# Performance work log

Hardware: AMD Instinct MI355X
Metric: run time of the kernel (lower is better)

## Reference

```python
import jax, jax.numpy as jnp
import numpy as np
from jax import lax

MODEL_DIM = 256
CTX_LEN = 48
CHUNK = 16
NUM_LAYERS = 4
NHEAD = 8
FF_DIM = 1024
EPS = 1e-5


def setup_inputs() -> dict:
    key = jax.random.key(0)
    ks = jax.random.split(key, 16)
    B, C, T = 16, MODEL_DIM, 1024
    s = 0.02
    inp = {
        "x": jax.random.normal(ks[0], (B, C, T), dtype=jnp.float32),
        "embedding": jax.random.normal(ks[1], (B, 2, C, 32), dtype=jnp.float32),
        "ctx_buf": jnp.zeros((B, NUM_LAYERS, CTX_LEN, C), dtype=jnp.float32),
        # per-layer stacked transformer-decoder-layer params
        "Wqkv": jax.random.normal(ks[2], (NUM_LAYERS, 3 * C, C), dtype=jnp.float32) * s,
        "bqkv": jnp.zeros((NUM_LAYERS, 3 * C), dtype=jnp.float32),
        "Wo": jax.random.normal(ks[3], (NUM_LAYERS, C, C), dtype=jnp.float32) * s,
        "bo": jnp.zeros((NUM_LAYERS, C), dtype=jnp.float32),
        "W1": jax.random.normal(ks[4], (NUM_LAYERS, FF_DIM, C), dtype=jnp.float32) * s,
        "b1": jnp.zeros((NUM_LAYERS, FF_DIM), dtype=jnp.float32),
        "W2": jax.random.normal(ks[5], (NUM_LAYERS, C, FF_DIM), dtype=jnp.float32) * s,
        "b2": jnp.zeros((NUM_LAYERS, C), dtype=jnp.float32),
        "ln1_g": jnp.ones((NUM_LAYERS, C), dtype=jnp.float32),
        "ln1_b": jnp.zeros((NUM_LAYERS, C), dtype=jnp.float32),
        "ln3_g": jnp.ones((NUM_LAYERS, C), dtype=jnp.float32),
        "ln3_b": jnp.zeros((NUM_LAYERS, C), dtype=jnp.float32),
    }
    return inp


def _layernorm(x, g, b):
    mu = jnp.mean(x, axis=-1, keepdims=True)
    var = jnp.mean(jnp.square(x - mu), axis=-1, keepdims=True)
    return (x - mu) * lax.rsqrt(var + EPS) * g + b


def _mha(q_in, kv_in, Wqkv, bqkv, Wo, bo):
    # q_in: [N, Lq, C], kv_in: [N, Lk, C]; torch nn.MultiheadAttention math (eval mode)
    C = q_in.shape[-1]
    dh = C // NHEAD
    Wq, Wk, Wv = jnp.split(Wqkv, 3, axis=0)
    bq, bk, bv = jnp.split(bqkv, 3)
    q = q_in @ Wq.T + bq
    k = kv_in @ Wk.T + bk
    v = kv_in @ Wv.T + bv
    N, Lq, _ = q.shape
    Lk = k.shape[1]
    q = q.reshape(N, Lq, NHEAD, dh)
    k = k.reshape(N, Lk, NHEAD, dh)
    v = v.reshape(N, Lk, NHEAD, dh)
    scores = jnp.einsum("nqhd,nkhd->nhqk", q, k) / jnp.sqrt(jnp.asarray(dh, q.dtype))
    attn = jax.nn.softmax(scores, axis=-1)
    out = jnp.einsum("nhqk,nkhd->nqhd", attn, v).reshape(N, Lq, C)
    return out @ Wo.T + bo


def _decoder_layer(tgt, Wqkv, bqkv, Wo, bo, W1, b1, W2, b2, ln1_g, ln1_b, ln3_g, ln3_b):
    # tgt: [N, ctx+chunk, C]; query = last `chunk` tokens; dropout=identity (eval)
    q = tgt[:, -CHUNK:, :]
    x1 = _layernorm(q + _mha(q, tgt, Wqkv, bqkv, Wo, bo), ln1_g, ln1_b)
    ff = jax.nn.relu(x1 @ W1.T + b1) @ W2.T + b2
    return _layernorm(x1 + ff, ln3_g, ln3_b)


def reference(x, embedding, ctx_buf, Wqkv, bqkv, Wo, bo, W1, b1, W2, b2,
              ln1_g, ln1_b, ln3_g, ln3_b):
    B, C, T = x.shape  # T multiple of CHUNK -> mod_pad is a no-op
    # ---- conv conditioning: per-(batch,channel) causal depthwise filter ----
    Le = embedding.shape[-1]
    filt = jnp.mean(embedding, axis=1).reshape(B * C, 1, Le)  # [B*C, 1, Le]
    inp = x.reshape(1, B * C, T)
    out = lax.conv_general_dilated(
        inp, filt, window_strides=(1,), padding=[(Le - 1, 0)],
        feature_group_count=B * C, dimension_numbers=("NCH", "OIH", "NCH"))
    output = out.reshape(B, C, T).transpose(0, 2, 1)  # [B, T, C]

    # ---- causal sliding-window decoder layers ----
    nwin = T // CHUNK
    W = CTX_LEN + CHUNK
    idx = jnp.arange(nwin)[:, None] * CHUNK + jnp.arange(W)[None, :]  # [nwin, W]
    for i in range(NUM_LAYERS):
        tgt_full = jnp.concatenate([ctx_buf[:, i], output], axis=1)  # [B, ctx+T, C]
        ctx_buf = ctx_buf.at[:, i].set(tgt_full[:, -CTX_LEN:])
        win = tgt_full[:, idx].reshape(B * nwin, W, C)  # unfold -> [B*nwin, W, C]
        chunks = _decoder_layer(win, Wqkv[i], bqkv[i], Wo[i], bo[i], W1[i], b1[i],
                                W2[i], b2[i], ln1_g[i], ln1_b[i], ln3_g[i], ln3_b[i])
        output = chunks.reshape(B, T, C)
    return output.transpose(0, 2, 1), ctx_buf
```

## Files before the change

### kernel.cpp

```cpp
#include <hip/hip_runtime.h>
#include <math.h>

#define BQ      16
#define CDIM    256
#define TLEN    1024
#define CTXL    48
#define CHUNKL  16
#define NLAYER  4
#define NHEADS  8
#define DHEAD   32
#define FFDIM   1024
#define NWIN    64
#define EXTL    1072
#define QKV_N   768

typedef __attribute__((ext_vector_type(4))) float floatx4;
typedef __attribute__((ext_vector_type(8))) __bf16 bf16x8;

__device__ __forceinline__ unsigned short f2bf(float f) {
    unsigned int u = __float_as_uint(f);
    u += 0x7fff + ((u >> 16) & 1);
    return (unsigned short)(u >> 16);
}
__device__ __forceinline__ float bf2f(unsigned short h) {
    return __uint_as_float(((unsigned int)h) << 16);
}

__global__ void f2b_kernel(const float* __restrict__ in,
                           unsigned short* __restrict__ out, int n) {
    int i = (blockIdx.x * 256 + threadIdx.x) * 4;
    if (i < n) {
        float4 v = *(const float4*)(in + i);
        ushort4 o;
        o.x = f2bf(v.x); o.y = f2bf(v.y); o.z = f2bf(v.z); o.w = f2bf(v.w);
        *(ushort4*)(out + i) = o;
    }
}

__global__ void conv_kernel(const float* __restrict__ x,
                            const float* __restrict__ emb,
                            float* __restrict__ tmp) {
    int bc = blockIdx.x;
    int b = bc >> 8, c = bc & 255;
    __shared__ float xs[31 + TLEN];
    __shared__ float f[32];
    int t = threadIdx.x;
    if (t < 31) xs[t] = 0.f;
    const float* xrow = x + (size_t)bc * TLEN;
    for (int s = t; s < TLEN; s += 256) xs[31 + s] = xrow[s];
    if (t < 32) {
        const float* e0 = emb + (((size_t)b * 2 + 0) * CDIM + c) * 32;
        const float* e1 = emb + (((size_t)b * 2 + 1) * CDIM + c) * 32;
        f[t] = 0.5f * (e0[t] + e1[t]);
    }
    __syncthreads();
    float* orow = tmp + (size_t)bc * TLEN;
    for (int s = t; s < TLEN; s += 256) {
        float acc = 0.f;
#pragma unroll
        for (int l = 0; l < 32; ++l) acc += f[l] * xs[s + l];
        orow[s] = acc;
    }
}

__global__ void transpose_f2b_kernel(const float* __restrict__ in,
                                     unsigned short* __restrict__ out,
                                     int R, int S) {
    __shared__ float tile[32][33];
    int b = blockIdx.z;
    int s0 = blockIdx.x * 32, r0 = blockIdx.y * 32;
    const float* inb = in + (size_t)b * R * S;
    unsigned short* outb = out + (size_t)b * R * S;
    int tx = threadIdx.x, ty = threadIdx.y;
    for (int i = ty; i < 32; i += 8)
        tile[i][tx] = inb[(size_t)(r0 + i) * S + s0 + tx];
    __syncthreads();
    for (int i = ty; i < 32; i += 8)
        outb[(size_t)(s0 + i) * R + r0 + tx] = f2bf(tile[tx][i]);
}

__global__ void transpose_b2f_kernel(const unsigned short* __restrict__ in,
                                     float* __restrict__ out,
                                     int R, int S) {
    __shared__ float tile[32][33];
    int b = blockIdx.z;
    int s0 = blockIdx.x * 32, r0 = blockIdx.y * 32;
    const unsigned short* inb = in + (size_t)b * R * S;
    float* outb = out + (size_t)b * R * S;
    int tx = threadIdx.x, ty = threadIdx.y;
    for (int i = ty; i < 32; i += 8)
        tile[i][tx] = bf2f(inb[(size_t)(r0 + i) * S + s0 + tx]);
    __syncthreads();
    for (int i = ty; i < 32; i += 8)
        outb[(size_t)(s0 + i) * R + r0 + tx] = tile[tx][i];
}

__global__ void ctx_copy_kernel(const unsigned short* __restrict__ act,
                                float* __restrict__ ctx_out, int layer) {
    int idx = blockIdx.x * 256 + threadIdx.x;
    int c = idx & 255;
    int r = (idx >> 8) % CTXL;
    int b = idx / (CTXL * CDIM);
    ctx_out[(((size_t)b * NLAYER + layer) * CTXL + r) * CDIM + c] =
        bf2f(act[((size_t)b * TLEN + (TLEN - CTXL) + r) * CDIM + c]);
}

template<int BM, int BN, int WM, int WN>
__global__ __launch_bounds__(256) void gemm_bf16_kernel(
    const unsigned short* __restrict__ A,
    const unsigned short* __restrict__ ctxb,
    int mode, int layer,
    const unsigned short* __restrict__ W,
    const float* __restrict__ bias,
    unsigned short* __restrict__ outb,
    int M, int N, int K, int relu) {
    constexpr int IA = BM / 32;
    constexpr int IB = BN / 32;
    constexpr int MT = WM / 16;
    constexpr int NTT = WN / 16;
    constexpr int NWX = BN / WN;
    __shared__ __align__(16) char smem[(BM + BN) * 128];
    char* smemA = smem;
    char* smemB = smem + BM * 128;
    int tid = threadIdx.x;
    int lane = tid & 63;
    int wid = tid >> 6;
    int ln = lane & 15, kq = lane >> 4;
    int wm = (wid / NWX) * WM, wn = (wid % NWX) * WN;
    int m0 = blockIdx.y * BM, n0 = blockIdx.x * BN;

    const unsigned short* arow[IA];
    int akc[IA];
    const unsigned short* brow[IB];
    int bkc[IB];
#pragma unroll
    for (int is = 0; is < IA; ++is) {
        int q = tid + is * 256;
        int m = q >> 3;
        akc[is] = ((q & 7) ^ (m & 7)) * 8;
        int mg = m0 + m;
        if (mode == 0) {
            arow[is] = A + (size_t)mg * K;
        } else {
            int b = mg / EXTL;
            int e = mg - b * EXTL;
            arow[is] = (e < CTXL)
                ? ctxb + (((size_t)b * NLAYER + layer) * CTXL + e) * CDIM
                : A + ((size_t)b * TLEN + (e - CTXL)) * CDIM;
        }
    }
#pragma unroll
    for (int is = 0; is < IB; ++is) {
        int q = tid + is * 256;
        int m = q >> 3;
        bkc[is] = ((q & 7) ^ (m & 7)) * 8;
        brow[is] = W + (size_t)(n0 + m) * K;
    }

    floatx4 acc[MT][NTT];
#pragma unroll
    for (int i = 0; i < MT; ++i)
#pragma unroll
        for (int j = 0; j < NTT; ++j) acc[i][j] = (floatx4){0.f, 0.f, 0.f, 0.f};

    for (int kt = 0; kt < K; kt += 64) {
#pragma unroll
        for (int is = 0; is < IA; ++is) {
            int off = (is * 256 + tid) * 16;
            __builtin_amdgcn_global_load_lds(
                (const __attribute__((address_space(1))) unsigned int*)
                    (const void*)(arow[is] + kt + akc[is]),
                (__attribute__((address_space(3))) unsigned int*)
                    (void*)(smemA + off), 16, 0, 0);
        }
#pragma unroll
        for (int is = 0; is < IB; ++is) {
            int off = (is * 256 + tid) * 16;
            __builtin_amdgcn_global_load_lds(
                (const __attribute__((address_space(1))) unsigned int*)
                    (const void*)(brow[is] + kt + bkc[is]),
                (__attribute__((address_space(3))) unsigned int*)
                    (void*)(smemB + off), 16, 0, 0);
        }
        __syncthreads();
#pragma unroll
        for (int s = 0; s < 2; ++s) {
            bf16x8 af[MT], bfv[NTT];
            int kc = s * 4 + kq;
#pragma unroll
            for (int i = 0; i < MT; ++i) {
                int ml = wm + 16 * i + ln;
                af[i] = *(const bf16x8*)(smemA + (ml * 8 + (kc ^ (ml & 7))) * 16);
            }
#pragma unroll
            for (int j = 0; j < NTT; ++j) {
                int nl = wn + 16 * j + ln;
                bfv[j] = *(const bf16x8*)(smemB + (nl * 8 + (kc ^ (nl & 7))) * 16);
            }
#pragma unroll
            for (int i = 0; i < MT; ++i)
#pragma unroll
                for (int j = 0; j < NTT; ++j)
                    acc[i][j] = __builtin_amdgcn_mfma_f32_16x16x32_bf16(
                        af[i], bfv[j], acc[i][j], 0, 0, 0);
        }
        __syncthreads();
    }

#pragma unroll
    for (int i = 0; i < MT; ++i) {
#pragma unroll
        for (int r = 0; r < 4; ++r) {
            int m = m0 + wm + 16 * i + kq * 4 + r;
#pragma unroll
            for (int j = 0; j < NTT; ++j) {
                int n = n0 + wn + 16 * j + ln;
                float v = acc[i][j][r] + bias[n];
                if (relu) v = fmaxf(v, 0.f);
                outb[(size_t)m * N + n] = f2bf(v);
            }
        }
    }
}

__global__ __launch_bounds__(256) void gemm_ln_kernel(
    const unsigned short* __restrict__ A,
    const unsigned short* __restrict__ W,
    const float* __restrict__ bias,
    const unsigned short* __restrict__ resid,
    const float* __restrict__ g,
    const float* __restrict__ beta,
    unsigned short* __restrict__ outb,
    int M, int K) {
    __shared__ __align__(16) unsigned short smA[32 * 64];
    __shared__ __align__(16) unsigned short smB[256 * 64];
    __shared__ float rsum[32][4];
    __shared__ float rsqs[32][4];
    int tid = threadIdx.x;
    int lane = tid & 63;
    int wid = tid >> 6;
    int ln = lane & 15, quad = lane >> 4;
    int wn = wid * 64;
    int m0 = blockIdx.x * 32;

    const unsigned short* arow =
        A + (size_t)(m0 + (tid >> 3)) * K + ((tid & 7) ^ ((tid >> 3) & 7)) * 8;
    const unsigned short* brow[8];
#pragma unroll
    for (int is = 0; is < 8; ++is) {
        int q = tid + is * 256;
        int mm = q >> 3;
        brow[is] = W + (size_t)mm * K + ((q & 7) ^ (mm & 7)) * 8;
    }

    floatx4 acc[2][4];
#pragma unroll
    for (int i = 0; i < 2; ++i)
#pragma unroll
        for (int j = 0; j < 4; ++j) acc[i][j] = (floatx4){0.f, 0.f, 0.f, 0.f};

    for (int kt = 0; kt < K; kt += 64) {
        __builtin_amdgcn_global_load_lds(
            (const __attribute__((address_space(1))) unsigned int*)
                (const void*)(arow + kt),
            (__attribute__((address_space(3))) unsigned int*)
                (void*)((char*)smA + tid * 16), 16, 0, 0);
#pragma unroll
        for (int is = 0; is < 8; ++is) {
            __builtin_amdgcn_global_load_lds(
                (const __attribute__((address_space(1))) unsigned int*)
                    (const void*)(brow[is] + kt),
                (__attribute__((address_space(3))) unsigned int*)
                    (void*)((char*)smB + (is * 256 + tid) * 16), 16, 0, 0);
        }
        __syncthreads();
#pragma unroll
        for (int s = 0; s < 2; ++s) {
            int kc = s * 4 + quad;
            bf16x8 af[2], bfv[4];
#pragma unroll
            for (int i = 0; i < 2; ++i) {
                int ml = 16 * i + ln;
                af[i] = *(const bf16x8*)(smA + (ml * 8 + (kc ^ (ml & 7))) * 8);
            }
#pragma unroll
            for (int j = 0; j < 4; ++j) {
                int nl = wn + 16 * j + ln;
                bfv[j] = *(const bf16x8*)(smB + (nl * 8 + (kc ^ (nl & 7))) * 8);
            }
#pragma unroll
            for (int i = 0; i < 2; ++i)
#pragma unroll
                for (int j = 0; j < 4; ++j)
                    acc[i][j] = __builtin_amdgcn_mfma_f32_16x16x32_bf16(
                        af[i], bfv[j], acc[i][j], 0, 0, 0);
        }
        __syncthreads();
    }

#pragma unroll
    for (int i = 0; i < 2; ++i)
#pragma unroll
        for (int r = 0; r < 4; ++r) {
            int m = m0 + 16 * i + quad * 4 + r;
#pragma unroll
            for (int j = 0; j < 4; ++j) {
                int n = wn + 16 * j + ln;
                acc[i][j][r] += bias[n] + bf2f(resid[(size_t)m * CDIM + n]);
            }
        }

#pragma unroll
    for (int i = 0; i < 2; ++i)
#pragma unroll
        for (int r = 0; r < 4; ++r) {
            float s1 = acc[i][0][r] + acc[i][1][r] + acc[i][2][r] + acc[i][3][r];
            float s2 = acc[i][0][r] * acc[i][0][r] + acc[i][1][r] * acc[i][1][r]
                     + acc[i][2][r] * acc[i][2][r] + acc[i][3][r] * acc[i][3][r];
#pragma unroll
            for (int off = 8; off >= 1; off >>= 1) {
                s1 += __shfl_xor(s1, off, 64);
                s2 += __shfl_xor(s2, off, 64);
            }
            if (ln == 0) {
                int row = 16 * i + quad * 4 + r;
                rsum[row][wid] = s1;
                rsqs[row][wid] = s2;
            }
        }
    __syncthreads();

#pragma unroll
    for (int i = 0; i < 2; ++i)
#pragma unroll
        for (int r = 0; r < 4; ++r) {
            int row = 16 * i + quad * 4 + r;
            float tot = rsum[row][0] + rsum[row][1] + rsum[row][2] + rsum[row][3];
            float tsq = rsqs[row][0] + rsqs[row][1] + rsqs[row][2] + rsqs[row][3];
            float mu = tot * (1.f / 256.f);
            float var = tsq * (1.f / 256.f) - mu * mu;
            float inv = rsqrtf(var + 1e-5f);
            int m = m0 + row;
#pragma unroll
            for (int j = 0; j < 4; ++j) {
                int n = wn + 16 * j + ln;
                float y = (acc[i][j][r] - mu) * inv * g[n] + beta[n];
                outb[(size_t)m * CDIM + n] = f2bf(y);
            }
        }
}

__global__ __launch_bounds__(256) void attn_mfma_kernel(
    const unsigned short* __restrict__ QKV,
    unsigned short* __restrict__ O) {
    int n = blockIdx.x, b = blockIdx.y;
    __shared__ __align__(16) unsigned short Vt[256][72];
    __shared__ __align__(16) unsigned short Pb[4][16][72];
    int tid = threadIdx.x;
    int lane = tid & 63, wid = tid >> 6;
    int ln = lane & 15, quad = lane >> 4;
    int key0 = n * CHUNKL;
    const unsigned short* base = QKV + (size_t)b * EXTL * QKV_N;

    {
        int row = tid >> 2;
        int c0 = (tid & 3) * 64;
        const unsigned short* vrow =
            base + (size_t)(key0 + row) * QKV_N + 512 + c0;
#pragma unroll
        for (int s = 0; s < 8; ++s) {
            bf16x8 v = *(const bf16x8*)(vrow + 8 * s);
#pragma unroll
            for (int j = 0; j < 8; ++j)
                Vt[c0 + 8 * s + j][row] = ((const unsigned short*)&v)[j];
        }
    }
    __syncthreads();

    const float scale = 0.17677669529663687f;
#pragma unroll
    for (int hh = 0; hh < 2; ++hh) {
        int h = wid * 2 + hh;
        bf16x8 qf = *(const bf16x8*)(base
            + (size_t)(CTXL + key0 + ln) * QKV_N + h * DHEAD + quad * 8);
        floatx4 sc[4];
#pragma unroll
        for (int j = 0; j < 4; ++j) {
            bf16x8 kf = *(const bf16x8*)(base
                + (size_t)(key0 + j * 16 + ln) * QKV_N + 256
                + h * DHEAD + quad * 8);
            sc[j] = __builtin_amdgcn_mfma_f32_16x16x32_bf16(
                qf, kf, (floatx4){0.f, 0.f, 0.f, 0.f}, 0, 0, 0);
        }
        float p[4][4];
#pragma unroll
        for (int r = 0; r < 4; ++r) {
            float mx = -1e30f;
#pragma unroll
            for (int j = 0; j < 4; ++j) mx = fmaxf(mx, sc[j][r]);
            mx = fmaxf(mx, __shfl_xor(mx, 1, 64));
            mx = fmaxf(mx, __shfl_xor(mx, 2, 64));
            mx = fmaxf(mx, __shfl_xor(mx, 4, 64));
            mx = fmaxf(mx, __shfl_xor(mx, 8, 64));
            float sum = 0.f;
#pragma unroll
            for (int j = 0; j < 4; ++j) {
                float e = __expf((sc[j][r] - mx) * scale);
                p[r][j] = e;
                sum += e;
            }
            sum += __shfl_xor(sum, 1, 64);
            sum += __shfl_xor(sum, 2, 64);
            sum += __shfl_xor(sum, 4, 64);
            sum += __shfl_xor(sum, 8, 64);
            float inv = 1.f / sum;
#pragma unroll
            for (int j = 0; j < 4; ++j) p[r][j] *= inv;
        }
#pragma unroll
        for (int r = 0; r < 4; ++r)
#pragma unroll
            for (int j = 0; j < 4; ++j)
                Pb[wid][quad * 4 + r][j * 16 + ln] = f2bf(p[r][j]);
        bf16x8 pa0 = *(const bf16x8*)&Pb[wid][ln][quad * 8];
        bf16x8 pa1 = *(const bf16x8*)&Pb[wid][ln][32 + quad * 8];
        floatx4 o[2];
#pragma unroll
        for (int jt = 0; jt < 2; ++jt) {
            bf16x8 v0 = *(const bf16x8*)&Vt[h * DHEAD + jt * 16 + ln][quad * 8];
            bf16x8 v1 = *(const bf16x8*)&Vt[h * DHEAD + jt * 16 + ln][32 + quad * 8];
            floatx4 a = __builtin_amdgcn_mfma_f32_16x16x32_bf16(
                pa0, v0, (floatx4){0.f, 0.f, 0.f, 0.f}, 0, 0, 0);
            o[jt] = __builtin_amdgcn_mfma_f32_16x16x32_bf16(pa1, v1, a, 0, 0, 0);
        }
        unsigned short* Ob =
            O + ((size_t)b * TLEN + n * CHUNKL) * CDIM + h * DHEAD;
#pragma unroll
        for (int jt = 0; jt < 2; ++jt)
#pragma unroll
            for (int r = 0; r < 4; ++r)
                Ob[(size_t)(quad * 4 + r) * CDIM + jt * 16 + ln] = f2bf(o[jt][r]);
    }
}

extern "C" void kernel_launch(void* const* d_in, const int* in_sizes, int n_in,
                              void* d_out, int out_size, void* d_ws, size_t ws_size,
                              hipStream_t stream) {
    const float* x    = (const float*)d_in[0];
    const float* emb  = (const float*)d_in[1];
    const float* ctx  = (const float*)d_in[2];
    const float* Wqkv = (const float*)d_in[3];
    const float* bqkv = (const float*)d_in[4];
    const float* Wo   = (const float*)d_in[5];
    const float* bo   = (const float*)d_in[6];
    const float* W1   = (const float*)d_in[7];
    const float* b1   = (const float*)d_in[8];
    const float* W2   = (const float*)d_in[9];
    const float* b2   = (const float*)d_in[10];
    const float* ln1g = (const float*)d_in[11];
    const float* ln1b = (const float*)d_in[12];
    const float* ln3g = (const float*)d_in[13];
    const float* ln3b = (const float*)d_in[14];

    float* out = (float*)d_out;
    float* ctx_out = out + (size_t)BQ * CDIM * TLEN;

    char* w = (char*)d_ws;
    float* convt = (float*)w;         w += 16777216;
    unsigned short* actbf  = (unsigned short*)w; w += 8388608;
    unsigned short* x1bf   = (unsigned short*)w; w += 8388608;
    unsigned short* Obf    = (unsigned short*)w; w += 8388608;
    unsigned short* QKVbf  = (unsigned short*)w; w += 26345472;
    unsigned short* Hbf    = (unsigned short*)w; w += 33554432;
    unsigned short* ctxbf  = (unsigned short*)w; w += 1572864;
    unsigned short* Wqkvbf = (unsigned short*)w; w += 1572864;
    unsigned short* Wobf   = (unsigned short*)w; w += 524288;
    unsigned short* W1bf   = (unsigned short*)w; w += 2097152;
    unsigned short* W2bf   = (unsigned short*)w; w += 2097152;

    const int NT = BQ * TLEN;

    f2b_kernel<<<768, 256, 0, stream>>>(Wqkv, Wqkvbf, NLAYER * 3 * CDIM * CDIM);
    f2b_kernel<<<256, 256, 0, stream>>>(Wo, Wobf, NLAYER * CDIM * CDIM);
    f2b_kernel<<<1024, 256, 0, stream>>>(W1, W1bf, NLAYER * FFDIM * CDIM);
    f2b_kernel<<<1024, 256, 0, stream>>>(W2, W2bf, NLAYER * CDIM * FFDIM);
    f2b_kernel<<<768, 256, 0, stream>>>(ctx, ctxbf, BQ * NLAYER * CTXL * CDIM);

    conv_kernel<<<BQ * CDIM, 256, 0, stream>>>(x, emb, convt);
    transpose_f2b_kernel<<<dim3(TLEN / 32, CDIM / 32, BQ), dim3(32, 8), 0,
                           stream>>>(convt, actbf, CDIM, TLEN);

    for (int i = 0; i < NLAYER; ++i) {
        const unsigned short* Wqkvb = Wqkvbf + (size_t)i * 3 * CDIM * CDIM;
        const float* bqi = bqkv + (size_t)i * 3 * CDIM;
        const unsigned short* Wob = Wobf + (size_t)i * CDIM * CDIM;
        const float* boi = bo + (size_t)i * CDIM;
        const unsigned short* W1b = W1bf + (size_t)i * FFDIM * CDIM;
        const float* b1i = b1 + (size_t)i * FFDIM;
        const unsigned short* W2b = W2bf + (size_t)i * CDIM * FFDIM;
        const float* b2i = b2 + (size_t)i * CDIM;

        ctx_copy_kernel<<<(BQ * CTXL * CDIM) / 256, 256, 0, stream>>>(
            actbf, ctx_out, i);
        gemm_bf16_kernel<128, 128, 64, 64><<<dim3(6, 134), 256, 0, stream>>>(
            actbf, ctxbf, 1, i, Wqkvb, bqi, QKVbf, BQ * EXTL, QKV_N, CDIM, 0);
        attn_mfma_kernel<<<dim3(NWIN, BQ), 256, 0, stream>>>(QKVbf, Obf);
        gemm_ln_kernel<<<NT / 32, 256, 0, stream>>>(
            Obf, Wob, boi, actbf, ln1g + i * CDIM, ln1b + i * CDIM,
            x1bf, NT, CDIM);
        gemm_bf16_kernel<128, 128, 64, 64><<<dim3(8, 128), 256, 0, stream>>>(
            x1bf, nullptr, 0, i, W1b, b1i, Hbf, NT, FFDIM, CDIM, 1);
        gemm_ln_kernel<<<NT / 32, 256, 0, stream>>>(
            Hbf, W2b, b2i, x1bf, ln3g + i * CDIM, ln3b + i * CDIM,
            actbf, NT, FFDIM);
    }

    transpose_b2f_kernel<<<dim3(CDIM / 32, TLEN / 32, BQ), dim3(32, 8), 0,
                           stream>>>(actbf, out, TLEN, CDIM);
}
```

Baseline: 504.7 us.

## Fuse attention with Wo projection and LayerNorm; fold ctx writes into producers

Attention output stays in shared memory and is multiplied by Wo inside the attention kernel, then bias, residual and LayerNorm are applied there. This removes the separate Obf buffer round-trip and one gemm_ln launch per layer. The context-buffer copy kernel is gone: the conv transpose and the FFN LayerNorm kernels now write the last 48 rows straight into ctx_out. The five weight-conversion launches are merged into one multi-segment kernel. In exchange, Wo fragments are read directly from global memory per block without shared staging, and the fused kernel uses only 1024 blocks with extra work each.

New measurement: 510.5 us. Within noise of the previous version (+1.1%).

```diff
diff --git a/kernel.cpp b/kernel.cpp
--- a/kernel.cpp
+++ b/kernel.cpp
@@ -26,14 +26,26 @@
     return __uint_as_float(((unsigned int)h) << 16);
 }
 
-__global__ void f2b_kernel(const float* __restrict__ in,
-                           unsigned short* __restrict__ out, int n) {
+__global__ void f2b_multi_kernel(const float* __restrict__ p0,
+                                 const float* __restrict__ p1,
+                                 const float* __restrict__ p2,
+                                 const float* __restrict__ p3,
+                                 const float* __restrict__ p4,
+                                 unsigned short* __restrict__ q0,
+                                 unsigned short* __restrict__ q1,
+                                 unsigned short* __restrict__ q2,
+                                 unsigned short* __restrict__ q3,
+                                 unsigned short* __restrict__ q4) {
+    const int sizes[5] = {786432, 262144, 1048576, 1048576, 786432};
+    const float* ins[5] = {p0, p1, p2, p3, p4};
+    unsigned short* outs[5] = {q0, q1, q2, q3, q4};
+    int seg = blockIdx.y;
     int i = (blockIdx.x * 256 + threadIdx.x) * 4;
-    if (i < n) {
-        float4 v = *(const float4*)(in + i);
+    if (i < sizes[seg]) {
+        float4 v = *(const float4*)(ins[seg] + i);
         ushort4 o;
         o.x = f2bf(v.x); o.y = f2bf(v.y); o.z = f2bf(v.z); o.w = f2bf(v.w);
-        *(ushort4*)(out + i) = o;
+        *(ushort4*)(outs[seg] + i) = o;
     }
 }
 
@@ -65,6 +77,7 @@
 
 __global__ void transpose_f2b_kernel(const float* __restrict__ in,
                                      unsigned short* __restrict__ out,
+                                     float* __restrict__ ctxo,
                                      int R, int S) {
     __shared__ float tile[32][33];
     int b = blockIdx.z;
@@ -75,8 +88,14 @@
     for (int i = ty; i < 32; i += 8)
         tile[i][tx] = inb[(size_t)(r0 + i) * S + s0 + tx];
     __syncthreads();
-    for (int i = ty; i < 32; i += 8)
-        outb[(size_t)(s0 + i) * R + r0 + tx] = f2bf(tile[tx][i]);
+    for (int i = ty; i < 32; i += 8) {
+        float v = tile[tx][i];
+        int t = s0 + i, c = r0 + tx;
+        outb[(size_t)t * R + c] = f2bf(v);
+        if (t >= TLEN - CTXL)
+            ctxo[(((size_t)b * NLAYER + 0) * CTXL + (t - (TLEN - CTXL)))
+                 * CDIM + c] = v;
+    }
 }
 
 __global__ void transpose_b2f_kernel(const unsigned short* __restrict__ in,
@@ -93,16 +112,6 @@
     __syncthreads();
     for (int i = ty; i < 32; i += 8)
         outb[(size_t)(s0 + i) * R + r0 + tx] = tile[tx][i];
-}
-
-__global__ void ctx_copy_kernel(const unsigned short* __restrict__ act,
-                                float* __restrict__ ctx_out, int layer) {
-    int idx = blockIdx.x * 256 + threadIdx.x;
-    int c = idx & 255;
-    int r = (idx >> 8) % CTXL;
-    int b = idx / (CTXL * CDIM);
-    ctx_out[(((size_t)b * NLAYER + layer) * CTXL + r) * CDIM + c] =
-        bf2f(act[((size_t)b * TLEN + (TLEN - CTXL) + r) * CDIM + c]);
 }
 
 template<int BM, int BN, int WM, int WN>
@@ -231,6 +240,7 @@
     const float* __restrict__ g,
     const float* __restrict__ beta,
     unsigned short* __restrict__ outb,
+    float* __restrict__ ctxo, int clayer,
     int M, int K) {
     __shared__ __align__(16) unsigned short smA[32 * 64];
     __shared__ __align__(16) unsigned short smB[256 * 64];
@@ -341,21 +351,34 @@
             float var = tsq * (1.f / 256.f) - mu * mu;
             float inv = rsqrtf(var + 1e-5f);
             int m = m0 + row;
+            int t = m & (TLEN - 1), bb = m >> 10;
+            bool wctx = (clayer >= 0) && (t >= TLEN - CTXL);
 #pragma unroll
             for (int j = 0; j < 4; ++j) {
                 int n = wn + 16 * j + ln;
                 float y = (acc[i][j][r] - mu) * inv * g[n] + beta[n];
                 outb[(size_t)m * CDIM + n] = f2bf(y);
-            }
-        }
-}
-
-__global__ __launch_bounds__(256) void attn_mfma_kernel(
+                if (wctx)
+                    ctxo[(((size_t)bb * NLAYER + clayer) * CTXL
+                          + (t - (TLEN - CTXL))) * CDIM + n] = y;
+            }
+        }
+}
+
+__global__ __launch_bounds__(256) void attn_wo_ln_kernel(
     const unsigned short* __restrict__ QKV,
-    unsigned short* __restrict__ O) {
+    const unsigned short* __restrict__ act,
+    const unsigned short* __restrict__ Wo,
+    const float* __restrict__ bo,
+    const float* __restrict__ g,
+    const float* __restrict__ beta,
+    unsigned short* __restrict__ x1out) {
     int n = blockIdx.x, b = blockIdx.y;
     __shared__ __align__(16) unsigned short Vt[256][72];
     __shared__ __align__(16) unsigned short Pb[4][16][72];
+    __shared__ __align__(16) unsigned short Ol[16][280];
+    __shared__ float rsum[16][4];
+    __shared__ float rsqs[16][4];
     int tid = threadIdx.x;
     int lane = tid & 63, wid = tid >> 6;
     int ln = lane & 15, quad = lane >> 4;
@@ -424,22 +447,79 @@
                 Pb[wid][quad * 4 + r][j * 16 + ln] = f2bf(p[r][j]);
         bf16x8 pa0 = *(const bf16x8*)&Pb[wid][ln][quad * 8];
         bf16x8 pa1 = *(const bf16x8*)&Pb[wid][ln][32 + quad * 8];
-        floatx4 o[2];
 #pragma unroll
         for (int jt = 0; jt < 2; ++jt) {
             bf16x8 v0 = *(const bf16x8*)&Vt[h * DHEAD + jt * 16 + ln][quad * 8];
             bf16x8 v1 = *(const bf16x8*)&Vt[h * DHEAD + jt * 16 + ln][32 + quad * 8];
             floatx4 a = __builtin_amdgcn_mfma_f32_16x16x32_bf16(
                 pa0, v0, (floatx4){0.f, 0.f, 0.f, 0.f}, 0, 0, 0);
-            o[jt] = __builtin_amdgcn_mfma_f32_16x16x32_bf16(pa1, v1, a, 0, 0, 0);
-        }
-        unsigned short* Ob =
-            O + ((size_t)b * TLEN + n * CHUNKL) * CDIM + h * DHEAD;
-#pragma unroll
-        for (int jt = 0; jt < 2; ++jt)
+            a = __builtin_amdgcn_mfma_f32_16x16x32_bf16(pa1, v1, a, 0, 0, 0);
+            int colb = wid * 64 + hh * 32 + jt * 16 + ln;
 #pragma unroll
             for (int r = 0; r < 4; ++r)
-                Ob[(size_t)(quad * 4 + r) * CDIM + jt * 16 + ln] = f2bf(o[jt][r]);
+                Ol[quad * 4 + r][colb] = f2bf(a[r]);
+        }
+    }
+    __syncthreads();
+
+    floatx4 o2[4];
+#pragma unroll
+    for (int j = 0; j < 4; ++j) o2[j] = (floatx4){0.f, 0.f, 0.f, 0.f};
+#pragma unroll
+    for (int s = 0; s < 8; ++s) {
+        bf16x8 af = *(const bf16x8*)&Ol[ln][s * 32 + quad * 8];
+#pragma unroll
+        for (int j = 0; j < 4; ++j) {
+            bf16x8 bv = *(const bf16x8*)(Wo
+                + (size_t)(wid * 64 + j * 16 + ln) * CDIM + s * 32 + quad * 8);
+            o2[j] = __builtin_amdgcn_mfma_f32_16x16x32_bf16(af, bv, o2[j], 0, 0, 0);
+        }
+    }
+
+    const unsigned short* residb =
+        act + ((size_t)b * TLEN + key0) * CDIM;
+#pragma unroll
+    for (int r = 0; r < 4; ++r) {
+        int row = quad * 4 + r;
+#pragma unroll
+        for (int j = 0; j < 4; ++j) {
+            int col = wid * 64 + j * 16 + ln;
+            o2[j][r] += bo[col] + bf2f(residb[(size_t)row * CDIM + col]);
+        }
+    }
+
+#pragma unroll
+    for (int r = 0; r < 4; ++r) {
+        float s1 = o2[0][r] + o2[1][r] + o2[2][r] + o2[3][r];
+        float s2 = o2[0][r] * o2[0][r] + o2[1][r] * o2[1][r]
+                 + o2[2][r] * o2[2][r] + o2[3][r] * o2[3][r];
+#pragma unroll
+        for (int off = 8; off >= 1; off >>= 1) {
+            s1 += __shfl_xor(s1, off, 64);
+            s2 += __shfl_xor(s2, off, 64);
+        }
+        if (ln == 0) {
+            rsum[quad * 4 + r][wid] = s1;
+            rsqs[quad * 4 + r][wid] = s2;
+        }
+    }
+    __syncthreads();
+
+    unsigned short* xout = x1out + ((size_t)b * TLEN + key0) * CDIM;
+#pragma unroll
+    for (int r = 0; r < 4; ++r) {
+        int row = quad * 4 + r;
+        float tot = rsum[row][0] + rsum[row][1] + rsum[row][2] + rsum[row][3];
+        float tsq = rsqs[row][0] + rsqs[row][1] + rsqs[row][2] + rsqs[row][3];
+        float mu = tot * (1.f / 256.f);
+        float var = tsq * (1.f / 256.f) - mu * mu;
+        float inv = rsqrtf(var + 1e-5f);
+#pragma unroll
+        for (int j = 0; j < 4; ++j) {
+            int col = wid * 64 + j * 16 + ln;
+            float y = (o2[j][r] - mu) * inv * g[col] + beta[col];
+            xout[(size_t)row * CDIM + col] = f2bf(y);
+        }
     }
 }
 
@@ -469,7 +549,6 @@
     float* convt = (float*)w;         w += 16777216;
     unsigned short* actbf  = (unsigned short*)w; w += 8388608;
     unsigned short* x1bf   = (unsigned short*)w; w += 8388608;
-    unsigned short* Obf    = (unsigned short*)w; w += 8388608;
     unsigned short* QKVbf  = (unsigned short*)w; w += 26345472;
     unsigned short* Hbf    = (unsigned short*)w; w += 33554432;
     unsigned short* ctxbf  = (unsigned short*)w; w += 1572864;
@@ -480,15 +559,12 @@
 
     const int NT = BQ * TLEN;
 
-    f2b_kernel<<<768, 256, 0, stream>>>(Wqkv, Wqkvbf, NLAYER * 3 * CDIM * CDIM);
-    f2b_kernel<<<256, 256, 0, stream>>>(Wo, Wobf, NLAYER * CDIM * CDIM);
-    f2b_kernel<<<1024, 256, 0, stream>>>(W1, W1bf, NLAYER * FFDIM * CDIM);
-    f2b_kernel<<<1024, 256, 0, stream>>>(W2, W2bf, NLAYER * CDIM * FFDIM);
-    f2b_kernel<<<768, 256, 0, stream>>>(ctx, ctxbf, BQ * NLAYER * CTXL * CDIM);
+    f2b_multi_kernel<<<dim3(1024, 5), 256, 0, stream>>>(
+        Wqkv, Wo, W1, W2, ctx, Wqkvbf, Wobf, W1bf, W2bf, ctxbf);
 
     conv_kernel<<<BQ * CDIM, 256, 0, stream>>>(x, emb, convt);
     transpose_f2b_kernel<<<dim3(TLEN / 32, CDIM / 32, BQ), dim3(32, 8), 0,
-                           stream>>>(convt, actbf, CDIM, TLEN);
+                           stream>>>(convt, actbf, ctx_out, CDIM, TLEN);
 
     for (int i = 0; i < NLAYER; ++i) {
         const unsigned short* Wqkvb = Wqkvbf + (size_t)i * 3 * CDIM * CDIM;
@@ -500,19 +576,15 @@
         const unsigned short* W2b = W2bf + (size_t)i * CDIM * FFDIM;
         const float* b2i = b2 + (size_t)i * CDIM;
 
-        ctx_copy_kernel<<<(BQ * CTXL * CDIM) / 256, 256, 0, stream>>>(
-            actbf, ctx_out, i);
         gemm_bf16_kernel<128, 128, 64, 64><<<dim3(6, 134), 256, 0, stream>>>(
             actbf, ctxbf, 1, i, Wqkvb, bqi, QKVbf, BQ * EXTL, QKV_N, CDIM, 0);
-        attn_mfma_kernel<<<dim3(NWIN, BQ), 256, 0, stream>>>(QKVbf, Obf);
-        gemm_ln_kernel<<<NT / 32, 256, 0, stream>>>(
-            Obf, Wob, boi, actbf, ln1g + i * CDIM, ln1b + i * CDIM,
-            x1bf, NT, CDIM);
+        attn_wo_ln_kernel<<<dim3(NWIN, BQ), 256, 0, stream>>>(
+            QKVbf, actbf, Wob, boi, ln1g + i * CDIM, ln1b + i * CDIM, x1bf);
         gemm_bf16_kernel<128, 128, 64, 64><<<dim3(8, 128), 256, 0, stream>>>(
             x1bf, nullptr, 0, i, W1b, b1i, Hbf, NT, FFDIM, CDIM, 1);
         gemm_ln_kernel<<<NT / 32, 256, 0, stream>>>(
             Hbf, W2b, b2i, x1bf, ln3g + i * CDIM, ln3b + i * CDIM,
-            actbf, NT, FFDIM);
+            actbf, ctx_out, (i < NLAYER - 1) ? (i + 1) : -1, NT, FFDIM);
     }
 
     transpose_b2f_kernel<<<dim3(CDIM / 32, TLEN / 32, BQ), dim3(32, 8), 0,
```
